# Optimization experiments

Measured on AMD Instinct MI355X. Metric: run time of the kernel, lower is better.

Reference implementation:

```python
import jax, jax.numpy as jnp
import numpy as np
from jax import lax

WINDOW_SIZE = 12
POOL = 4  # AvgPool2d(4): 12x12 -> 3x3

# 4 directional 3x3 kernels, stacked as [O=4, I=1, 3, 3]
_KERNELS = np.stack([
    np.array([[0, 0, 0], [-1, 1, 0], [0, 0, 0]], np.float32),  # left
    np.array([[0, 0, 0], [0, 1, -1], [0, 0, 0]], np.float32),  # right
    np.array([[0, -1, 0], [0, 1, 0], [0, 0, 0]], np.float32),  # up
    np.array([[0, 0, 0], [0, 1, 0], [0, -1, 0]], np.float32),  # down
])[:, None, :, :]


def setup_inputs() -> dict:
    key = jax.random.key(0)
    k1, k2 = jax.random.split(key)
    windows_num = 200000
    n = WINDOW_SIZE * WINDOW_SIZE * windows_num
    samples1 = jax.random.uniform(k1, (n, 3), dtype=jnp.float32)
    samples2 = jax.random.uniform(k2, (n, 3), dtype=jnp.float32)
    return {"samples1": samples1, "samples2": samples2, "windows_num": windows_num}


def _to_pooled(samples, windows_num):
    # [W*W*N, C] -> [W, W, N, C] -> [N, C, W, W]
    x = samples.reshape(WINDOW_SIZE, WINDOW_SIZE, windows_num, -1)
    x = jnp.transpose(x, (2, 3, 0, 1))
    # channel mean, keepdim -> [N, 1, W, W]
    m = jnp.mean(x, axis=1, keepdims=True)
    # AvgPool2d(4): [N,1,12,12] -> [N,1,3,3]
    hp = WINDOW_SIZE // POOL
    p = m.reshape(windows_num, 1, hp, POOL, hp, POOL).mean(axis=(3, 5))
    return p


def _dir_grads(x):
    # x: [N,1,3,3]; 4 directional 3x3 convs, padding=1 -> [N,4,3,3]
    k = jnp.asarray(_KERNELS)
    return lax.conv_general_dilated(
        x, k, window_strides=(1, 1), padding=[(1, 1), (1, 1)],
        dimension_numbers=("NCHW", "OIHW", "NCHW"))


def reference(samples1, samples2, windows_num):
    org_pool = _to_pooled(samples1, windows_num)
    enh_pool = _to_pooled(samples2, windows_num)
    d_org = _dir_grads(org_pool)
    d_enh = _dir_grads(enh_pool)
    # squared diff per direction, summed over the 4 directions -> [N,3,3]
    E = jnp.sum((d_org - d_enh) ** 2, axis=1)
    return jnp.mean(E)
```

## Files before the change

### kernel.cpp

```cpp
#include <hip/hip_runtime.h>

__global__ __launch_bounds__(256) void spa_kernel(
    const float* __restrict__ s1, const float* __restrict__ s2,
    float* __restrict__ out, int N, float scale) {
  int n = blockIdx.x * blockDim.x + threadIdx.x;

  float D[9];
#pragma unroll
  for (int k = 0; k < 9; ++k) D[k] = 0.f;

  if (n < N) {
    const size_t stride = (size_t)N * 3u;
    const float* p1 = s1 + (size_t)n * 3u;
    const float* p2 = s2 + (size_t)n * 3u;
    for (int i = 0; i < 12; ++i) {
      const int pi = (i >> 2) * 3;
      const float* q1 = p1 + (size_t)(i * 12) * stride;
      const float* q2 = p2 + (size_t)(i * 12) * stride;
#pragma unroll
      for (int j = 0; j < 12; ++j) {
        const float* a = q1 + (size_t)j * stride;
        const float* b = q2 + (size_t)j * stride;
        float d = (a[0] + a[1] + a[2]) - (b[0] + b[1] + b[2]);
        D[pi + (j >> 2)] += d;
      }
    }
  }

  const float inv48 = 1.0f / 48.0f;
  float P[9];
#pragma unroll
  for (int k = 0; k < 9; ++k) P[k] = D[k] * inv48;

  float e = 0.f;
#pragma unroll
  for (int i = 0; i < 3; ++i) {
#pragma unroll
    for (int j = 0; j < 3; ++j) {
      float c = P[i * 3 + j];
      float l = (j > 0) ? P[i * 3 + j - 1] : 0.f;
      float r = (j < 2) ? P[i * 3 + j + 1] : 0.f;
      float u = (i > 0) ? P[(i - 1) * 3 + j] : 0.f;
      float d = (i < 2) ? P[(i + 1) * 3 + j] : 0.f;
      float dl = c - l, dr = c - r, du = c - u, dd = c - d;
      e += dl * dl + dr * dr + du * du + dd * dd;
    }
  }

#pragma unroll
  for (int off = 32; off > 0; off >>= 1) e += __shfl_down(e, off, 64);
  __shared__ float sm[4];
  int lane = threadIdx.x & 63;
  int wid = threadIdx.x >> 6;
  if (lane == 0) sm[wid] = e;
  __syncthreads();
  if (threadIdx.x == 0) {
    atomicAdd(out, (sm[0] + sm[1] + sm[2] + sm[3]) * scale);
  }
}

extern "C" void kernel_launch(void* const* d_in, const int* in_sizes, int n_in,
                              void* d_out, int out_size, void* d_ws, size_t ws_size,
                              hipStream_t stream) {
  const float* s1 = (const float*)d_in[0];
  const float* s2 = (const float*)d_in[1];
  float* out = (float*)d_out;
  int N = in_sizes[0] / (12 * 12 * 3);
  float scale = 1.0f / (9.0f * (float)N);
  hipMemsetAsync(d_out, 0, sizeof(float), stream);
  int blocks = (N + 255) / 256;
  spa_kernel<<<blocks, 256, 0, stream>>>(s1, s2, out, N, scale);
}
```

Before: 653.2 us.

## Split each window's pixel rows across four wavefronts with shared-memory combine

Each block now handles 64 windows, and each of its four wavefronts accumulates a different 3-row slice of the 12x12 window. Partial row sums go through shared memory, and one wavefront builds the pooled 3x3 grid and computes the gradient energy. This shortens each thread's serial load chain and puts more independent loads in flight per window, at the cost of a shared-memory round trip, a barrier, and four times as many blocks and atomics.

Measured after the change: 618.2 us. 5.4% less time.

```diff
diff --git a/kernel.cpp b/kernel.cpp
--- a/kernel.cpp
+++ b/kernel.cpp
@@ -3,18 +3,23 @@
 __global__ __launch_bounds__(256) void spa_kernel(
     const float* __restrict__ s1, const float* __restrict__ s2,
     float* __restrict__ out, int N, float scale) {
-  int n = blockIdx.x * blockDim.x + threadIdx.x;
+  const int lane = threadIdx.x & 63;
+  const int rg   = threadIdx.x >> 6;
+  const int win  = blockIdx.x * 64 + lane;
 
-  float D[9];
+  float rowacc[3][3];
 #pragma unroll
-  for (int k = 0; k < 9; ++k) D[k] = 0.f;
+  for (int a = 0; a < 3; ++a)
+#pragma unroll
+    for (int b = 0; b < 3; ++b) rowacc[a][b] = 0.f;
 
-  if (n < N) {
+  if (win < N) {
     const size_t stride = (size_t)N * 3u;
-    const float* p1 = s1 + (size_t)n * 3u;
-    const float* p2 = s2 + (size_t)n * 3u;
-    for (int i = 0; i < 12; ++i) {
-      const int pi = (i >> 2) * 3;
+    const float* p1 = s1 + (size_t)win * 3u;
+    const float* p2 = s2 + (size_t)win * 3u;
+#pragma unroll
+    for (int ii = 0; ii < 3; ++ii) {
+      const int i = rg * 3 + ii;
       const float* q1 = p1 + (size_t)(i * 12) * stride;
       const float* q2 = p2 + (size_t)(i * 12) * stride;
 #pragma unroll
@@ -22,40 +27,49 @@
         const float* a = q1 + (size_t)j * stride;
         const float* b = q2 + (size_t)j * stride;
         float d = (a[0] + a[1] + a[2]) - (b[0] + b[1] + b[2]);
-        D[pi + (j >> 2)] += d;
+        rowacc[ii][j >> 2] += d;
       }
     }
   }
 
-  const float inv48 = 1.0f / 48.0f;
-  float P[9];
+  __shared__ float sRow[12][64][3];
 #pragma unroll
-  for (int k = 0; k < 9; ++k) P[k] = D[k] * inv48;
+  for (int ii = 0; ii < 3; ++ii) {
+    const int i = rg * 3 + ii;
+#pragma unroll
+    for (int c = 0; c < 3; ++c) sRow[i][lane][c] = rowacc[ii][c];
+  }
+  __syncthreads();
 
-  float e = 0.f;
+  if (rg == 0) {
+    float P[9];
 #pragma unroll
-  for (int i = 0; i < 3; ++i) {
+    for (int p = 0; p < 3; ++p)
 #pragma unroll
-    for (int j = 0; j < 3; ++j) {
-      float c = P[i * 3 + j];
-      float l = (j > 0) ? P[i * 3 + j - 1] : 0.f;
-      float r = (j < 2) ? P[i * 3 + j + 1] : 0.f;
-      float u = (i > 0) ? P[(i - 1) * 3 + j] : 0.f;
-      float d = (i < 2) ? P[(i + 1) * 3 + j] : 0.f;
-      float dl = c - l, dr = c - r, du = c - u, dd = c - d;
-      e += dl * dl + dr * dr + du * du + dd * dd;
+      for (int c = 0; c < 3; ++c) {
+        float v = sRow[4 * p][lane][c] + sRow[4 * p + 1][lane][c] +
+                  sRow[4 * p + 2][lane][c] + sRow[4 * p + 3][lane][c];
+        P[p * 3 + c] = v * (1.0f / 48.0f);
+      }
+
+    float e = 0.f;
+#pragma unroll
+    for (int i = 0; i < 3; ++i) {
+#pragma unroll
+      for (int j = 0; j < 3; ++j) {
+        float c = P[i * 3 + j];
+        float l = (j > 0) ? P[i * 3 + j - 1] : 0.f;
+        float r = (j < 2) ? P[i * 3 + j + 1] : 0.f;
+        float u = (i > 0) ? P[(i - 1) * 3 + j] : 0.f;
+        float d = (i < 2) ? P[(i + 1) * 3 + j] : 0.f;
+        float dl = c - l, dr = c - r, du = c - u, dd = c - d;
+        e += dl * dl + dr * dr + du * du + dd * dd;
+      }
     }
-  }
 
 #pragma unroll
-  for (int off = 32; off > 0; off >>= 1) e += __shfl_down(e, off, 64);
-  __shared__ float sm[4];
-  int lane = threadIdx.x & 63;
-  int wid = threadIdx.x >> 6;
-  if (lane == 0) sm[wid] = e;
-  __syncthreads();
-  if (threadIdx.x == 0) {
-    atomicAdd(out, (sm[0] + sm[1] + sm[2] + sm[3]) * scale);
+    for (int off = 32; off > 0; off >>= 1) e += __shfl_down(e, off, 64);
+    if (lane == 0) atomicAdd(out, e * scale);
   }
 }
 
@@ -68,6 +82,6 @@
   int N = in_sizes[0] / (12 * 12 * 3);
   float scale = 1.0f / (9.0f * (float)N);
   hipMemsetAsync(d_out, 0, sizeof(float), stream);
-  int blocks = (N + 255) / 256;
+  int blocks = (N + 63) / 64;
   spa_kernel<<<blocks, 256, 0, stream>>>(s1, s2, out, N, scale);
 }
```
